# Optimization experiments

Hardware: AMD Instinct MI355X
Metric: run time of the kernel (lower is better)

## Reference

```python
import jax, jax.numpy as jnp
import numpy as np

E = 1024   # embed_dim
H = 16     # num_heads
HD = E // H
T, B, S = 1024, 4, 1024


def setup_inputs() -> dict:
    key = jax.random.key(0)
    ks = jax.random.split(key, 6)
    g = lambda k, sh, sc=1.0: jax.random.normal(k, sh, dtype=jnp.float32) * sc
    return {
        "query": g(ks[0], (T, B, E)),
        "key": g(ks[1], (S, B, E)),
        "value": g(ks[2], (S, B, E)),
        "in_proj_weight": g(ks[3], (3 * E, E), E ** -0.5),
        "in_proj_bias": jnp.zeros((3 * E,), jnp.float32),
        "out_w": g(ks[4], (E, E), E ** -0.5),
        "out_b": jnp.zeros((E,), jnp.float32),
    }


def reference(query, key, value, in_proj_weight, in_proj_bias, out_w, out_b):
    # qkv not same and kv not same -> decorr=True cross-attention branch.
    W, b = in_proj_weight, in_proj_bias
    scaling = HD ** -0.5
    half = E // 2
    # Note: original uses F.linear(x, weight_slice.T, bias) == x @ weight_slice + bias
    q = query @ W[:E] + b[:E]                       # [T,B,E]
    k = key @ W[E:2 * E] + b[E:2 * E]               # [S,B,E]
    Wv = W[2 * E:]                                  # [E,E] V block
    v_corr = value @ Wv[:, :half] + b[2 * E:2 * E + half]      # [S,B,E/2]
    v_decorr = value @ Wv[:, half:] + b[2 * E + half:]         # [S,B,E/2]
    q = q * scaling
    # heads: [T,B,E] -> [B*H, T, hd]; per-branch V has head_dim/2 per head
    qh = q.reshape(T, B * H, HD).transpose(1, 0, 2)
    kh = k.reshape(S, B * H, HD).transpose(1, 0, 2)
    vch = v_corr.reshape(S, B * H, HD // 2).transpose(1, 0, 2)
    vdh = v_decorr.reshape(S, B * H, HD // 2).transpose(1, 0, 2)
    scores = jnp.einsum('btd,bsd->bts', qh, kh)     # [B*H, T, S]
    a_corr = jax.nn.softmax(scores, axis=-1)
    a_decorr = jax.nn.softmax(-scores, axis=-1)     # softmin(x) = softmax(-x)
    # dropout p=0.0 (eval) -> identity
    attn = jnp.concatenate([
        jnp.einsum('bts,bsd->btd', a_corr, vch),
        jnp.einsum('bts,bsd->btd', a_decorr, vdh),
    ], axis=-1)                                     # [B*H, T, HD]
    attn = attn.transpose(1, 0, 2).reshape(T, B, E)
    attn = attn @ out_w.T + out_b                   # nn.Linear out_proj
    # returned attn_weights are the RAW (pre-softmax) scores averaged over heads
    avg_w = scores.reshape(B, H, T, S).sum(axis=1) / H
    return attn, avg_w
```

## Files before the change

### kernel.cpp

```cpp
#include <hip/hip_runtime.h>
#include <hip/hip_bf16.h>


typedef __bf16 bf16;
typedef float f32x4 __attribute__((ext_vector_type(4)));
typedef float float4v __attribute__((ext_vector_type(4)));
typedef bf16 bf16x8 __attribute__((ext_vector_type(8)));
typedef bf16 bf16x4 __attribute__((ext_vector_type(4)));

#define LOG2E 1.4426950408889634f

__device__ __forceinline__ void gll16(const void* g, void* l) {
  __builtin_amdgcn_global_load_lds(
      (const __attribute__((address_space(1))) void*)g,
      (__attribute__((address_space(3))) void*)l, 16, 0, 0);
}

__device__ __forceinline__ int xcd_swz(int flat, int nwg) {
  int q = nwg >> 3;
  return (flat & 7) * q + (flat >> 3);
}

__device__ __forceinline__ bf16x4 cvt4(float4v v) {
  bf16x4 b = { (bf16)v.x, (bf16)v.y, (bf16)v.z, (bf16)v.w };
  return b;
}

__global__ __launch_bounds__(256) void prep_all(
    const float* __restrict__ W, const float* __restrict__ out_w,
    bf16* __restrict__ WT, bf16* __restrict__ owb) {
  __shared__ bf16 tile[64][72];
  int bid = blockIdx.x;
  if (bid >= 768) {
    int i = ((bid - 768) * 256 + (int)threadIdx.x) * 4;
    float4v v = *(const float4v*)(out_w + i);
    *(bf16x4*)&owb[i] = cvt4(v);
    return;
  }
  int sec = bid >> 8, bx = bid & 15, by = (bid >> 4) & 15;
  int i0 = by * 64, j0 = bx * 64;
  const float* s = W + (long)sec * 1048576;
  bf16* d = WT + (long)sec * 1048576;
  int t = threadIdx.x;
#pragma unroll
  for (int p = 0; p < 4; p++) {
    int ri = (t >> 4) + p * 16, cj = (t & 15) * 4;
    float4v vv = *(const float4v*)(s + (long)(i0 + ri) * 1024 + j0 + cj);
    *(bf16x4*)&tile[ri][cj] = cvt4(vv);
  }
  __syncthreads();
#pragma unroll
  for (int p = 0; p < 4; p++) {
    int rj = (t >> 4) + p * 16, ci = (t & 15) * 4;
    bf16x4 bv = { tile[ci][rj], tile[ci + 1][rj], tile[ci + 2][rj], tile[ci + 3][rj] };
    *(bf16x4*)&d[(long)(j0 + rj) * 1024 + i0 + ci] = bv;
  }
}

template <bool AF32>
__device__ __forceinline__ void gemm_core(
    const void* __restrict__ Av, long lda,
    const bf16* __restrict__ B, long ldb,
    void* __restrict__ C, long ldc,
    const float* __restrict__ bias, float scale, int K,
    int m0, int n0, int cmode) {
  __shared__ bf16 smem[16384];
  bf16 (*sA)[4096] = (bf16(*)[4096])smem;
  bf16 (*sB)[4096] = (bf16(*)[4096])(smem + 8192);
  int t = threadIdx.x;
  int w = t >> 6, lane = t & 63, r = lane & 15, g = lane >> 4;
  int mq = (w >> 1) * 32, nq = (w & 1) * 64;
  int srow = w * 16 + (lane >> 2);
  int scol = ((lane & 3) ^ ((srow >> 1) & 3)) * 8;
  int fsw = (r >> 1) & 3;
  const bf16* Bs = B + (long)(n0 + srow) * ldb + scol;
  const bf16* As = (const bf16*)Av + (long)(m0 + srow) * lda + scol;
  int arow = t >> 3, acol = (t & 7) * 4;
  const float* Af0 = (const float*)Av + (long)(m0 + arow) * lda + acol;
  const float* Af1 = (const float*)Av + (long)(m0 + arow + 64) * lda + acol;
  int aoff0 = arow * 32 + 8 * ((acol >> 3) ^ ((arow >> 1) & 3)) + (acol & 4);
  int aoff1 = (arow + 64) * 32 + 8 * ((acol >> 3) ^ (((arow + 64) >> 1) & 3)) + (acol & 4);

  f32x4 acc[2][4];
#pragma unroll
  for (int mi = 0; mi < 2; mi++)
#pragma unroll
    for (int ni = 0; ni < 4; ni++) acc[mi][ni] = (f32x4){0.f, 0.f, 0.f, 0.f};

  if (AF32) {
    *(bf16x4*)&sA[0][aoff0] = cvt4(*(const float4v*)Af0);
    *(bf16x4*)&sA[0][aoff1] = cvt4(*(const float4v*)Af1);
  } else {
    gll16(As, &sA[0][w * 512]);
  }
  gll16(Bs, &sB[0][w * 512]);
  __syncthreads();
  int cur = 0;
  for (int k0 = 0; k0 < K; k0 += 32) {
    float4v a0n, a1n;
    if (k0 + 32 < K) {
      if (AF32) {
        a0n = *(const float4v*)(Af0 + k0 + 32);
        a1n = *(const float4v*)(Af1 + k0 + 32);
      } else {
        gll16(As + k0 + 32, &sA[cur ^ 1][w * 512]);
      }
      gll16(Bs + k0 + 32, &sB[cur ^ 1][w * 512]);
    }
    bf16x8 af[2], bfr[4];
#pragma unroll
    for (int mi = 0; mi < 2; mi++)
      af[mi] = *(bf16x8*)&sA[cur][(mq + mi * 16 + r) * 32 + 8 * (g ^ fsw)];
#pragma unroll
    for (int ni = 0; ni < 4; ni++)
      bfr[ni] = *(bf16x8*)&sB[cur][(nq + ni * 16 + r) * 32 + 8 * (g ^ fsw)];
#pragma unroll
    for (int mi = 0; mi < 2; mi++)
#pragma unroll
      for (int ni = 0; ni < 4; ni++)
        acc[mi][ni] = __builtin_amdgcn_mfma_f32_16x16x32_bf16(af[mi], bfr[ni], acc[mi][ni], 0, 0, 0);
    if (AF32 && k0 + 32 < K) {
      *(bf16x4*)&sA[cur ^ 1][aoff0] = cvt4(a0n);
      *(bf16x4*)&sA[cur ^ 1][aoff1] = cvt4(a1n);
    }
    __syncthreads();
    cur ^= 1;
  }

  if (cmode == 3) {
#pragma unroll
    for (int mi = 0; mi < 2; mi++) {
      int s32 = (mq >> 2) + mi * 4 + g;
      int gq = (s32 >> 2) & 3;
      int u = ((s32 >> 4) << 2) | (s32 & 3);
#pragma unroll
      for (int ni = 0; ni < 4; ni++) {
        int col = n0 + nq + ni * 16 + r;
        float bv = bias ? bias[col] : 0.f;
        int clbase = ((nq >> 5) + (ni >> 1)) * 2 + (ni & 1);
#pragma unroll
        for (int j = 0; j < 4; j++) {
          float val = (acc[mi][ni][j] + bv) * scale;
          smem[(j * 8 + clbase) * 512 + (gq * 16 + r) * 8 + u] = (bf16)val;
        }
      }
    }
    __syncthreads();
    int sc_ = m0 >> 7;
    int hh0 = (n0 & 511) >> 5;
    int half = n0 >> 9;
#pragma unroll
    for (int c = 0; c < 4; c++) {
      int cl = w * 4 + c;
      int b_ = cl >> 3, hl = (cl >> 1) & 3, dl = cl & 1;
      long chunk = ((long)(b_ * 16 + hh0 + hl) * 32 + sc_) * 4 + half * 2 + dl;
      bf16x8 v = *(bf16x8*)&smem[cl * 512 + lane * 8];
      *(bf16x8*)&((bf16*)C)[(chunk << 9) + lane * 8] = v;
    }
    return;
  }

#pragma unroll
  for (int mi = 0; mi < 2; mi++)
#pragma unroll
    for (int ni = 0; ni < 4; ni++) {
      int col = n0 + nq + ni * 16 + r;
      float bv = bias ? bias[col] : 0.f;
#pragma unroll
      for (int j = 0; j < 4; j++) {
        int row = m0 + mq + mi * 16 + g * 4 + j;
        float val = (acc[mi][ni][j] + bv) * scale;
        if (cmode == 2) {
          int bb = row & 3, tt = row >> 2, hh = col >> 6, dd = col & 63;
          ((bf16*)C)[((long)(bb * 16 + hh) * 1024 + tt) * 64 + dd] = (bf16)val;
        } else if (cmode == 1) {
          ((bf16*)C)[(long)row * ldc + col] = (bf16)val;
        } else {
          ((float*)C)[(long)row * ldc + col] = val;
        }
      }
    }
}

__global__ __launch_bounds__(512) void gemm_out(
    const bf16* __restrict__ A, const bf16* __restrict__ B,
    float* __restrict__ C, const float* __restrict__ bias) {
  int nwg = gridDim.x * gridDim.y;
  int flat = blockIdx.x + gridDim.x * blockIdx.y;
  int work = xcd_swz(flat, nwg);
  int n = work % gridDim.x, m = work / gridDim.x;
  gemm_core<false>(A, 1024, B, 1024, C, 1024, bias, 1.0f, 1024, m * 128, n * 128, 0);
}

__global__ __launch_bounds__(512) void gemm_proj(
    const float* __restrict__ q, const float* __restrict__ k,
    const float* __restrict__ v, const bf16* __restrict__ WT,
    const float* __restrict__ bias, bf16* __restrict__ qkout,
    bf16* __restrict__ vf) {
  int nwg = gridDim.x * gridDim.y * gridDim.z;
  int flat = blockIdx.x + gridDim.x * (blockIdx.y + gridDim.y * blockIdx.z);
  int work = xcd_swz(flat, nwg);
  int n = work % gridDim.x;
  int m = (work / gridDim.x) % gridDim.y;
  int z = work / (gridDim.x * gridDim.y);
  const float* A = (z == 0) ? q : ((z == 1) ? k : v);
  const bf16* B = WT + (long)z * 1048576;
  const float* bz = bias + z * 1024;
  void* C = (z == 2) ? (void*)vf : (void*)(qkout + (long)z * 4194304);
  float scale = (z == 0) ? 0.125f * LOG2E : 1.0f;
  gemm_core<true>(A, 1024, B, 1024, C, 1024, bz, scale, 1024, m * 128, n * 128,
                  z == 2 ? 3 : 2);
}

__global__ __launch_bounds__(512) void gemm_avg(
    const bf16* __restrict__ qh, const bf16* __restrict__ kh,
    float* __restrict__ out, float scale) {
  __shared__ bf16 sA[2][4096];
  __shared__ bf16 sB[2][4096];
  int nwg = gridDim.x * gridDim.y * gridDim.z;
  int flat = blockIdx.x + gridDim.x * (blockIdx.y + gridDim.y * blockIdx.z);
  int work = xcd_swz(flat, nwg);
  int n0 = (work % gridDim.x) * 128;
  int m0 = ((work / gridDim.x) % gridDim.y) * 128;
  int bb = work / (gridDim.x * gridDim.y);
  int t = threadIdx.x;
  int w = t >> 6, lane = t & 63, r = lane & 15, g = lane >> 4;
  int mq = (w >> 1) * 32, nq = (w & 1) * 64;
  int srow = w * 16 + (lane >> 2);
  int scol = ((lane & 3) ^ ((srow >> 1) & 3)) * 8;
  int fsw = (r >> 1) & 3;
  const bf16* As = qh + (long)bb * 1048576 + (long)(m0 + srow) * 64 + scol;
  const bf16* Bs = kh + (long)bb * 1048576 + (long)(n0 + srow) * 64 + scol;

  f32x4 acc[2][4];
#pragma unroll
  for (int mi = 0; mi < 2; mi++)
#pragma unroll
    for (int ni = 0; ni < 4; ni++) acc[mi][ni] = (f32x4){0.f, 0.f, 0.f, 0.f};

  gll16(As, &sA[0][w * 512]);
  gll16(Bs, &sB[0][w * 512]);
  __syncthreads();
  int cur = 0;
  for (int k0 = 0; k0 < 1024; k0 += 32) {
    if (k0 + 32 < 1024) {
      int kn = k0 + 32;
      long off = ((long)(kn >> 6)) * 65536 + (kn & 63);
      gll16(As + off, &sA[cur ^ 1][w * 512]);
      gll16(Bs + off, &sB[cur ^ 1][w * 512]);
    }
    bf16x8 af[2], bfr[4];
#pragma unroll
    for (int mi = 0; mi < 2; mi++)
      af[mi] = *(bf16x8*)&sA[cur][(mq + mi * 16 + r) * 32 + 8 * (g ^ fsw)];
#pragma unroll
    for (int ni = 0; ni < 4; ni++)
      bfr[ni] = *(bf16x8*)&sB[cur][(nq + ni * 16 + r) * 32 + 8 * (g ^ fsw)];
#pragma unroll
    for (int mi = 0; mi < 2; mi++)
#pragma unroll
      for (int ni = 0; ni < 4; ni++)
        acc[mi][ni] = __builtin_amdgcn_mfma_f32_16x16x32_bf16(af[mi], bfr[ni], acc[mi][ni], 0, 0, 0);
    __syncthreads();
    cur ^= 1;
  }

#pragma unroll
  for (int mi = 0; mi < 2; mi++)
#pragma unroll
    for (int ni = 0; ni < 4; ni++) {
      int col = n0 + nq + ni * 16 + r;
#pragma unroll
      for (int j = 0; j < 4; j++) {
        int row = m0 + mq + mi * 16 + g * 4 + j;
        out[(long)bb * 1048576 + (long)row * 1024 + col] = acc[mi][ni][j] * scale;
      }
    }
}

__global__ __launch_bounds__(256) void attn_fused(
    const bf16* __restrict__ qh, const bf16* __restrict__ kh,
    const bf16* __restrict__ vf, bf16* __restrict__ attn_b) {
  __shared__ bf16 sK[2][4096];
  __shared__ bf16 sV[2][4096];
  int bh = blockIdx.x;
  int b = bh >> 4, h = bh & 15;
  int t0 = blockIdx.y * 64;
  int tid = threadIdx.x, w = tid >> 6, lane = tid & 63, r = lane & 15, g = lane >> 4;
  int tw = t0 + w * 16;

  const bf16* qrow = qh + ((long)bh * 1024 + tw + r) * 64;
  bf16x8 aq0 = *(const bf16x8*)(qrow + g * 8);
  bf16x8 aq1 = *(const bf16x8*)(qrow + 32 + g * 8);

  float sp_acc = 0.f, sn_acc = 0.f;
  f32x4 o[4];
#pragma unroll
  for (int d = 0; d < 4; d++) o[d] = (f32x4){0.f, 0.f, 0.f, 0.f};

  const bf16* kbh = kh + (long)bh * 65536;
  const bf16* vbh = vf + (long)bh * 65536;

  int krow = w * 16 + (lane >> 3);
  const bf16* ksrc = kbh + (long)krow * 64 + 8 * ((lane & 7) ^ (krow & 7));
  const bf16* vsrc = vbh + w * 1024 + lane * 8;
  int c0 = 8 * (g ^ (r & 7));
  int c1 = 8 * ((g + 4) ^ (r & 7));

  auto stage = [&](int buf, int st) {
    const bf16* kp = ksrc + st * 4096;
    gll16(kp, &sK[buf][w * 1024]);
    gll16(kp + 512, &sK[buf][w * 1024 + 512]);
    const bf16* vp = vsrc + st * 4096;
    gll16(vp, &sV[buf][w * 1024]);
    gll16(vp + 512, &sV[buf][w * 1024 + 512]);
  };
  stage(0, 0);
  __syncthreads();
  int cur = 0;
#pragma unroll 1
  for (int st = 0; st < 16; st++) {
    if (st < 15) stage(cur ^ 1, st + 1);
    f32x4 sc4[4];
#pragma unroll
    for (int sf = 0; sf < 4; sf++) {
      int row = sf * 16 + r;
      bf16x8 k0 = *(const bf16x8*)&sK[cur][row * 64 + c0];
      bf16x8 k1 = *(const bf16x8*)&sK[cur][row * 64 + c1];
      f32x4 z = (f32x4){0.f, 0.f, 0.f, 0.f};
      z = __builtin_amdgcn_mfma_f32_16x16x32_bf16(k0, aq0, z, 0, 0, 0);
      z = __builtin_amdgcn_mfma_f32_16x16x32_bf16(k1, aq1, z, 0, 0, 0);
      sc4[sf] = z;
    }
    bf16x8 pP[2], pN[2];
#pragma unroll
    for (int sf = 0; sf < 4; sf++)
#pragma unroll
      for (int j = 0; j < 4; j++) {
        float e = __builtin_amdgcn_exp2f(sc4[sf][j]);
        sp_acc += e;
        pP[sf >> 1][(sf & 1) * 4 + j] = (bf16)e;
        float f = __builtin_amdgcn_exp2f(-sc4[sf][j]);
        sn_acc += f;
        pN[sf >> 1][(sf & 1) * 4 + j] = (bf16)f;
      }
#pragma unroll
    for (int c = 0; c < 2; c++)
#pragma unroll
      for (int dblk = 0; dblk < 4; dblk++) {
        bf16x8 vv = *(const bf16x8*)&sV[cur][(c * 4 + dblk) * 512 + lane * 8];
        o[dblk] = __builtin_amdgcn_mfma_f32_16x16x32_bf16(
            vv, (dblk < 2) ? pP[c] : pN[c], o[dblk], 0, 0, 0);
      }
    __syncthreads();
    cur ^= 1;
  }

  sp_acc += __shfl_xor(sp_acc, 16); sp_acc += __shfl_xor(sp_acc, 32);
  sn_acc += __shfl_xor(sn_acc, 16); sn_acc += __shfl_xor(sn_acc, 32);
  float rlp = 1.f / sp_acc, rln = 1.f / sn_acc;
  long obase = ((long)(tw + r) * 4 + b) * 1024 + h * 64;
#pragma unroll
  for (int dblk = 0; dblk < 4; dblk++) {
    float rl = (dblk < 2) ? rlp : rln;
    bf16x4 ov;
#pragma unroll
    for (int j = 0; j < 4; j++) ov[j] = (bf16)(o[dblk][j] * rl);
    *(bf16x4*)&attn_b[obase + (dblk >> 1) * 32 + (dblk & 1) * 16 + g * 4] = ov;
  }
}

extern "C" void kernel_launch(void* const* d_in, const int* in_sizes, int n_in,
                              void* d_out, int out_size, void* d_ws, size_t ws_size,
                              hipStream_t stream) {
  (void)in_sizes; (void)n_in; (void)out_size; (void)ws_size;
  const float* query = (const float*)d_in[0];
  const float* key   = (const float*)d_in[1];
  const float* value = (const float*)d_in[2];
  const float* W     = (const float*)d_in[3];
  const float* bias  = (const float*)d_in[4];
  const float* out_w = (const float*)d_in[5];
  const float* out_b = (const float*)d_in[6];

  char* ws = (char*)d_ws;
  const long MB = 1 << 20;
  bf16* qh  = (bf16*)(ws + 0 * MB);
  bf16* kh  = (bf16*)(ws + 8 * MB);
  bf16* vf  = (bf16*)(ws + 24 * MB);
  bf16* ab  = (bf16*)(ws + 32 * MB);
  bf16* WT  = (bf16*)(ws + 40 * MB);
  bf16* owb = (bf16*)(ws + 46 * MB);
  float* out_attn = (float*)d_out;
  float* out_avg  = (float*)d_out + (size_t)4 * 1024 * 1024;

  prep_all<<<dim3(1792), 256, 0, stream>>>(W, out_w, WT, owb);

  gemm_proj<<<dim3(8, 32, 3), 512, 0, stream>>>(query, key, value, WT, bias, qh, vf);

  gemm_avg<<<dim3(8, 8, 4), 512, 0, stream>>>(qh, kh, out_avg,
                                              1.f / (16.f * LOG2E));

  attn_fused<<<dim3(64, 16), 256, 0, stream>>>(qh, kh, vf, ab);

  gemm_out<<<dim3(8, 32), 512, 0, stream>>>(ab, owb, out_attn, out_b);
}
```

Baseline: 126.0 us.

## Merge head-averaged score GEMM into attention kernel as extra blocks

The separate head-averaged score GEMM and the fused attention kernel become one launch. Blocks 0-1023 run attention and blocks 1024-1535 compute the avg-weight GEMM with 64x128 tiles at 256 threads. The aim is to cut one launch and let the two independent workloads run on the GPU at the same time, filling idle CUs. In exchange, the GEMM tiles are smaller and less efficient, and both branches share a 32KB shared-memory allocation that may limit occupancy.

Measured after the change: 112.8 us. -10.5%, faster.

```diff
diff --git a/kernel.cpp b/kernel.cpp
--- a/kernel.cpp
+++ b/kernel.cpp
@@ -212,81 +212,81 @@
                   z == 2 ? 3 : 2);
 }
 
-__global__ __launch_bounds__(512) void gemm_avg(
+__global__ __launch_bounds__(256) void attn_avg(
     const bf16* __restrict__ qh, const bf16* __restrict__ kh,
-    float* __restrict__ out, float scale) {
-  __shared__ bf16 sA[2][4096];
-  __shared__ bf16 sB[2][4096];
-  int nwg = gridDim.x * gridDim.y * gridDim.z;
-  int flat = blockIdx.x + gridDim.x * (blockIdx.y + gridDim.y * blockIdx.z);
-  int work = xcd_swz(flat, nwg);
-  int n0 = (work % gridDim.x) * 128;
-  int m0 = ((work / gridDim.x) % gridDim.y) * 128;
-  int bb = work / (gridDim.x * gridDim.y);
-  int t = threadIdx.x;
-  int w = t >> 6, lane = t & 63, r = lane & 15, g = lane >> 4;
-  int mq = (w >> 1) * 32, nq = (w & 1) * 64;
-  int srow = w * 16 + (lane >> 2);
-  int scol = ((lane & 3) ^ ((srow >> 1) & 3)) * 8;
+    const bf16* __restrict__ vf, bf16* __restrict__ attn_b,
+    float* __restrict__ out_avg, float avg_scale) {
+  __shared__ __align__(16) bf16 smem[16384];
+  int tid = threadIdx.x, w = tid >> 6, lane = tid & 63, r = lane & 15, g = lane >> 4;
   int fsw = (r >> 1) & 3;
-  const bf16* As = qh + (long)bb * 1048576 + (long)(m0 + srow) * 64 + scol;
-  const bf16* Bs = kh + (long)bb * 1048576 + (long)(n0 + srow) * 64 + scol;
-
-  f32x4 acc[2][4];
-#pragma unroll
-  for (int mi = 0; mi < 2; mi++)
-#pragma unroll
-    for (int ni = 0; ni < 4; ni++) acc[mi][ni] = (f32x4){0.f, 0.f, 0.f, 0.f};
-
-  gll16(As, &sA[0][w * 512]);
-  gll16(Bs, &sB[0][w * 512]);
-  __syncthreads();
-  int cur = 0;
-  for (int k0 = 0; k0 < 1024; k0 += 32) {
-    if (k0 + 32 < 1024) {
-      int kn = k0 + 32;
-      long off = ((long)(kn >> 6)) * 65536 + (kn & 63);
-      gll16(As + off, &sA[cur ^ 1][w * 512]);
-      gll16(Bs + off, &sB[cur ^ 1][w * 512]);
-    }
-    bf16x8 af[2], bfr[4];
+
+  if (blockIdx.x >= 1024) {
+    bf16* sA = smem;
+    bf16* sB = smem + 4096;
+    int work = xcd_swz(blockIdx.x - 1024, 512);
+    int n0 = (work & 7) * 128;
+    int m0 = ((work >> 3) & 15) * 64;
+    int bb = work >> 7;
+    int mq = (w >> 1) * 32, nq = (w & 1) * 64;
+    int srow = w * 16 + (lane >> 2);
+    int scol = ((lane & 3) ^ ((srow >> 1) & 3)) * 8;
+    const bf16* Asb = qh + (long)bb * 1048576 + (long)(m0 + srow) * 64 + scol;
+    const bf16* Bs0 = kh + (long)bb * 1048576 + (long)(n0 + srow) * 64 + scol;
+    const bf16* Bs1 = kh + (long)bb * 1048576 + (long)(n0 + srow + 64) * 64 + scol;
+
+    f32x4 acc[2][4];
 #pragma unroll
     for (int mi = 0; mi < 2; mi++)
-      af[mi] = *(bf16x8*)&sA[cur][(mq + mi * 16 + r) * 32 + 8 * (g ^ fsw)];
-#pragma unroll
-    for (int ni = 0; ni < 4; ni++)
-      bfr[ni] = *(bf16x8*)&sB[cur][(nq + ni * 16 + r) * 32 + 8 * (g ^ fsw)];
+#pragma unroll
+      for (int ni = 0; ni < 4; ni++) acc[mi][ni] = (f32x4){0.f, 0.f, 0.f, 0.f};
+
+    auto stage = [&](int buf, long off) {
+      gll16(Asb + off, &sA[buf * 2048 + w * 512]);
+      gll16(Bs0 + off, &sB[buf * 4096 + w * 512]);
+      gll16(Bs1 + off, &sB[buf * 4096 + 2048 + w * 512]);
+    };
+    stage(0, 0);
+    __syncthreads();
+    int cur = 0;
+    for (int k0 = 0; k0 < 1024; k0 += 32) {
+      if (k0 + 32 < 1024) {
+        int kn = k0 + 32;
+        stage(cur ^ 1, ((long)(kn >> 6)) * 65536 + (kn & 63));
+      }
+      bf16x8 af[2], bfr[4];
+#pragma unroll
+      for (int mi = 0; mi < 2; mi++)
+        af[mi] = *(bf16x8*)&sA[cur * 2048 + (mq + mi * 16 + r) * 32 + 8 * (g ^ fsw)];
+#pragma unroll
+      for (int ni = 0; ni < 4; ni++)
+        bfr[ni] = *(bf16x8*)&sB[cur * 4096 + (nq + ni * 16 + r) * 32 + 8 * (g ^ fsw)];
+#pragma unroll
+      for (int mi = 0; mi < 2; mi++)
+#pragma unroll
+        for (int ni = 0; ni < 4; ni++)
+          acc[mi][ni] = __builtin_amdgcn_mfma_f32_16x16x32_bf16(af[mi], bfr[ni], acc[mi][ni], 0, 0, 0);
+      __syncthreads();
+      cur ^= 1;
+    }
 #pragma unroll
     for (int mi = 0; mi < 2; mi++)
 #pragma unroll
-      for (int ni = 0; ni < 4; ni++)
-        acc[mi][ni] = __builtin_amdgcn_mfma_f32_16x16x32_bf16(af[mi], bfr[ni], acc[mi][ni], 0, 0, 0);
-    __syncthreads();
-    cur ^= 1;
-  }
-
-#pragma unroll
-  for (int mi = 0; mi < 2; mi++)
-#pragma unroll
-    for (int ni = 0; ni < 4; ni++) {
-      int col = n0 + nq + ni * 16 + r;
-#pragma unroll
-      for (int j = 0; j < 4; j++) {
-        int row = m0 + mq + mi * 16 + g * 4 + j;
-        out[(long)bb * 1048576 + (long)row * 1024 + col] = acc[mi][ni][j] * scale;
-      }
-    }
-}
-
-__global__ __launch_bounds__(256) void attn_fused(
-    const bf16* __restrict__ qh, const bf16* __restrict__ kh,
-    const bf16* __restrict__ vf, bf16* __restrict__ attn_b) {
-  __shared__ bf16 sK[2][4096];
-  __shared__ bf16 sV[2][4096];
-  int bh = blockIdx.x;
+      for (int ni = 0; ni < 4; ni++) {
+        int col = n0 + nq + ni * 16 + r;
+#pragma unroll
+        for (int j = 0; j < 4; j++) {
+          int row = m0 + mq + mi * 16 + g * 4 + j;
+          out_avg[(long)bb * 1048576 + (long)row * 1024 + col] = acc[mi][ni][j] * avg_scale;
+        }
+      }
+    return;
+  }
+
+  bf16* sK = smem;
+  bf16* sV = smem + 8192;
+  int bh = blockIdx.x & 63;
   int b = bh >> 4, h = bh & 15;
-  int t0 = blockIdx.y * 64;
-  int tid = threadIdx.x, w = tid >> 6, lane = tid & 63, r = lane & 15, g = lane >> 4;
+  int t0 = (blockIdx.x >> 6) * 64;
   int tw = t0 + w * 16;
 
   const bf16* qrow = qh + ((long)bh * 1024 + tw + r) * 64;
@@ -309,11 +309,11 @@
 
   auto stage = [&](int buf, int st) {
     const bf16* kp = ksrc + st * 4096;
-    gll16(kp, &sK[buf][w * 1024]);
-    gll16(kp + 512, &sK[buf][w * 1024 + 512]);
+    gll16(kp, &sK[buf * 4096 + w * 1024]);
+    gll16(kp + 512, &sK[buf * 4096 + w * 1024 + 512]);
     const bf16* vp = vsrc + st * 4096;
-    gll16(vp, &sV[buf][w * 1024]);
-    gll16(vp + 512, &sV[buf][w * 1024 + 512]);
+    gll16(vp, &sV[buf * 4096 + w * 1024]);
+    gll16(vp + 512, &sV[buf * 4096 + w * 1024 + 512]);
   };
   stage(0, 0);
   __syncthreads();
@@ -325,8 +325,8 @@
 #pragma unroll
     for (int sf = 0; sf < 4; sf++) {
       int row = sf * 16 + r;
-      bf16x8 k0 = *(const bf16x8*)&sK[cur][row * 64 + c0];
-      bf16x8 k1 = *(const bf16x8*)&sK[cur][row * 64 + c1];
+      bf16x8 k0 = *(const bf16x8*)&sK[cur * 4096 + row * 64 + c0];
+      bf16x8 k1 = *(const bf16x8*)&sK[cur * 4096 + row * 64 + c1];
       f32x4 z = (f32x4){0.f, 0.f, 0.f, 0.f};
       z = __builtin_amdgcn_mfma_f32_16x16x32_bf16(k0, aq0, z, 0, 0, 0);
       z = __builtin_amdgcn_mfma_f32_16x16x32_bf16(k1, aq1, z, 0, 0, 0);
@@ -348,7 +348,7 @@
     for (int c = 0; c < 2; c++)
 #pragma unroll
       for (int dblk = 0; dblk < 4; dblk++) {
-        bf16x8 vv = *(const bf16x8*)&sV[cur][(c * 4 + dblk) * 512 + lane * 8];
+        bf16x8 vv = *(const bf16x8*)&sV[cur * 4096 + (c * 4 + dblk) * 512 + lane * 8];
         o[dblk] = __builtin_amdgcn_mfma_f32_16x16x32_bf16(
             vv, (dblk < 2) ? pP[c] : pN[c], o[dblk], 0, 0, 0);
       }
@@ -397,10 +397,8 @@
 
   gemm_proj<<<dim3(8, 32, 3), 512, 0, stream>>>(query, key, value, WT, bias, qh, vf);
 
-  gemm_avg<<<dim3(8, 8, 4), 512, 0, stream>>>(qh, kh, out_avg,
-                                              1.f / (16.f * LOG2E));
-
-  attn_fused<<<dim3(64, 16), 256, 0, stream>>>(qh, kh, vf, ab);
+  attn_avg<<<dim3(1536), 256, 0, stream>>>(qh, kh, vf, ab, out_avg,
+                                           1.f / (16.f * LOG2E));
 
   gemm_out<<<dim3(8, 32), 512, 0, stream>>>(ab, owb, out_attn, out_b);
 }
```
